# Performance work log

Hardware: AMD Instinct MI355X
Metric: run time of the kernel (lower is better)

## Reference

```python
import jax, jax.numpy as jnp
import numpy as np

B, S, H, NH = 4, 2048, 1024, 16
D = H // NH  # head dim = 64


def setup_inputs() -> dict:
    key = jax.random.key(0)
    ks = jax.random.split(key, 4)
    scale = 1.0 / np.sqrt(H)
    return {
        "hidden_states": jax.random.normal(ks[0], (B, S, H), dtype=jnp.float32),
        "attention_mask": jnp.zeros((B, 1, 1, S), dtype=jnp.float32),
        "Wq": jax.random.normal(ks[1], (H, H), dtype=jnp.float32) * scale,
        "bq": jnp.zeros((H,), dtype=jnp.float32),
        "Wk": jax.random.normal(ks[2], (H, H), dtype=jnp.float32) * scale,
        "bk": jnp.zeros((H,), dtype=jnp.float32),
        "Wv": jax.random.normal(ks[3], (H, H), dtype=jnp.float32) * scale,
        "bv": jnp.zeros((H,), dtype=jnp.float32),
    }


def _split_heads(x):
    # [B, S, H] -> [B, NH, S, D]
    return x.reshape(B, S, NH, D).transpose(0, 2, 1, 3)


def reference(hidden_states, attention_mask, Wq, bq, Wk, bk, Wv, bv):
    # NOTE: faithful to source quirk: key/value projections are applied to the
    # query projection output (mixed_query_layer), not to keyvalue_states.
    mixed_q = hidden_states @ Wq.T + bq            # [B, S, H]
    q = _split_heads(mixed_q)                       # [B, NH, S, D]
    k = _split_heads(mixed_q @ Wk.T + bk)           # [B, NH, S, D]
    v = _split_heads(mixed_q @ Wv.T + bv)           # [B, NH, S, D]

    scores = jnp.einsum("bhqd,bhkd->bhqk", q, k) / jnp.sqrt(jnp.float32(D))
    scores = scores + attention_mask                # additive mask [B,1,1,S]
    probs = jax.nn.softmax(scores, axis=-1)         # dropout = identity (eval)
    ctx = jnp.einsum("bhqk,bhkd->bhqd", probs, v)   # [B, NH, S, D]
    ctx = ctx.transpose(0, 2, 1, 3).reshape(B, S, H)
    return ctx
```

## Files before the change

### kernel.cpp

```cpp
#include <hip/hip_runtime.h>
#include <stdint.h>

typedef float  f32x4  __attribute__((ext_vector_type(4)));
typedef float  f32x16 __attribute__((ext_vector_type(16)));
typedef short  s16x8  __attribute__((ext_vector_type(8)));
typedef unsigned int u32x4 __attribute__((ext_vector_type(4)));
typedef unsigned short u16;
typedef u16    u16x4 __attribute__((ext_vector_type(4)));

#define SLEN 2048
#define HDIM 1024
#define NHEAD 16
#define DHEAD 64
#define BATCH 4
#define LOG2E 1.44269504088896340736f
#define SC2   0.18033688011111772f
#define ISC2  5.5451774444795623f

__device__ __forceinline__ u16 f2bf(float f) {
  uint32_t u = __builtin_bit_cast(uint32_t, f);
  u += 0x7FFFu + ((u >> 16) & 1u);
  return (u16)(u >> 16);
}

__device__ __forceinline__ uint32_t cvtpk2(float a, float b) {
  uint32_t r;
  asm("v_cvt_pk_bf16_f32 %0, %1, %2" : "=v"(r) : "v"(a), "v"(b));
  return r;
}

__device__ __forceinline__ void gld_lds16(const void* g, void* l) {
  __builtin_amdgcn_global_load_lds(
      (const __attribute__((address_space(1))) unsigned int*)g,
      (__attribute__((address_space(3))) unsigned int*)l, 16, 0, 0);
}

__global__ __launch_bounds__(256) void cvt_bf16(const float4* __restrict__ in,
                                                u16* __restrict__ out, int n4) {
  int i = blockIdx.x * 256 + threadIdx.x;
  if (i < n4) {
    float4 v = in[i];
    u16x4 o;
    o.x = f2bf(v.x); o.y = f2bf(v.y); o.z = f2bf(v.z); o.w = f2bf(v.w);
    *(u16x4*)(out + (size_t)i * 4) = o;
  }
}

__global__ __launch_bounds__(256) void cvt_w3(const float4* __restrict__ W0,
                                              const float4* __restrict__ W1,
                                              const float4* __restrict__ W2,
                                              u16* __restrict__ O0,
                                              u16* __restrict__ O1,
                                              u16* __restrict__ O2) {
  const float4* in = blockIdx.y == 0 ? W0 : (blockIdx.y == 1 ? W1 : W2);
  u16* out = blockIdx.y == 0 ? O0 : (blockIdx.y == 1 ? O1 : O2);
  const float sc = blockIdx.y == 0 ? SC2 : ISC2;
  int i = blockIdx.x * 256 + threadIdx.x;
  float4 v = in[i];
  u16x4 o;
  o.x = f2bf(v.x * sc); o.y = f2bf(v.y * sc);
  o.z = f2bf(v.z * sc); o.w = f2bf(v.w * sc);
  *(u16x4*)(out + (size_t)i * 4) = o;
}

__global__ __launch_bounds__(256) void prep_small(const float* __restrict__ mask,
                                                  const float* __restrict__ bq,
                                                  float* __restrict__ m2,
                                                  float* __restrict__ bqs) {
  int bid = blockIdx.x, tid = threadIdx.x;
  if (bid < 32) {
    int i = bid * 256 + tid;
    m2[i] = mask[i] * LOG2E;
  } else {
#pragma unroll
    for (int k = 0; k < 4; ++k) bqs[tid + k * 256] = bq[tid + k * 256] * SC2;
  }
}

__device__ __forceinline__ void gemm_body(const u16* __restrict__ A,
                                          const u16* __restrict__ W,
                                          const float* __restrict__ bias,
                                          u16* __restrict__ C, int mode) {
  __shared__ u16 As[128][32];
  __shared__ u16 Bs[128][32];
  const int tid = threadIdx.x;
  const int lane = tid & 63;
  const int w = tid >> 6;
  const int wr = w >> 1, wc = w & 1;
  const int brow = blockIdx.y * 128;
  const int bcol = blockIdx.x * 128;
  const int l15 = lane & 15, l4 = lane >> 4;
  const int koff = l4 * 8;

  f32x4 acc[4][4];
#pragma unroll
  for (int m = 0; m < 4; ++m)
#pragma unroll
    for (int n = 0; n < 4; ++n) acc[m][n] = f32x4{0.f, 0.f, 0.f, 0.f};

  for (int kt = 0; kt < HDIM / 32; ++kt) {
    __syncthreads();
#pragma unroll
    for (int it = 0; it < 2; ++it) {
      int c = tid + it * 256;
      int r = c >> 2, c4 = c & 3;
      gld_lds16(A + (size_t)(brow + r) * HDIM + kt * 32 + c4 * 8,
                (u16*)&As[0][0] + (size_t)c * 8);
      gld_lds16(W + (size_t)(bcol + r) * HDIM + kt * 32 + c4 * 8,
                (u16*)&Bs[0][0] + (size_t)c * 8);
    }
    __syncthreads();

    s16x8 af[4], bfr[4];
#pragma unroll
    for (int m = 0; m < 4; ++m)
      af[m] = *(const s16x8*)&As[wr * 64 + m * 16 + l15][koff];
#pragma unroll
    for (int n = 0; n < 4; ++n)
      bfr[n] = *(const s16x8*)&Bs[wc * 64 + n * 16 + l15][koff];
#pragma unroll
    for (int m = 0; m < 4; ++m)
#pragma unroll
      for (int n = 0; n < 4; ++n)
        acc[m][n] = __builtin_amdgcn_mfma_f32_16x16x32_bf16(af[m], bfr[n],
                                                            acc[m][n], 0, 0, 0);
  }

#pragma unroll
  for (int n = 0; n < 4; ++n) {
    int col = bcol + wc * 64 + n * 16 + l15;
    float bv = bias[col];
#pragma unroll
    for (int m = 0; m < 4; ++m) {
      int row0 = brow + wr * 64 + m * 16 + l4 * 4;
      if (mode == 0) {
#pragma unroll
        for (int j = 0; j < 4; ++j)
          C[(size_t)(row0 + j) * HDIM + col] = f2bf(acc[m][n][j] + bv);
      } else {
        u16x4 o;
#pragma unroll
        for (int j = 0; j < 4; ++j) o[j] = f2bf(acc[m][n][j] + bv);
        *(u16x4*)(C + (size_t)(((row0 >> 11) << 10) + col) * SLEN +
                  (row0 & (SLEN - 1))) = o;
      }
    }
  }
}

__global__ __launch_bounds__(256) void gemm_bt(const u16* __restrict__ A,
                                               const u16* __restrict__ W,
                                               const float* __restrict__ bias,
                                               u16* __restrict__ C) {
  gemm_body(A, W, bias, C, 0);
}

__global__ __launch_bounds__(256) void gemm_kv(const u16* __restrict__ A,
                                               const u16* __restrict__ Wk,
                                               const float* __restrict__ bk,
                                               u16* __restrict__ K,
                                               const u16* __restrict__ Wv,
                                               const float* __restrict__ bv,
                                               u16* __restrict__ Vt) {
  if (blockIdx.z == 0) gemm_body(A, Wk, bk, K, 0);
  else                 gemm_body(A, Wv, bv, Vt, 1);
}

__global__ __launch_bounds__(256, 4) void attn_kernel(
    const u16* __restrict__ Qs, const u16* __restrict__ Kb,
    const u16* __restrict__ Vtg, const float* __restrict__ m2g,
    float* __restrict__ out) {
  __shared__ u16 Ks[2][64 * 64];
  __shared__ u16 Vts[2][64 * 64];

  const int tid = threadIdx.x;
  const int lane = tid & 63;
  const int w = tid >> 6;
  const int bid = blockIdx.x;
  const int swz = (bid & 7) * 128 + (bid >> 3);
  const int qt = swz & 15;
  const int bh = swz >> 4;
  const int b = bh >> 4, h = bh & 15;
  const int l31 = lane & 31;
  const int h1 = lane >> 5;

  const int q0 = qt * 128 + w * 32;
  s16x8 qf[4];
  {
    const u16* qp = Qs + (size_t)(b * SLEN + q0 + l31) * HDIM + h * DHEAD + h1 * 8;
#pragma unroll
    for (int dch = 0; dch < 4; ++dch) qf[dch] = *(const s16x8*)(qp + dch * 16);
  }

  const int r0 = tid >> 3, c0 = tid & 7;
  const int cl0 = c0 ^ (r0 & 7);
  const int r1 = r0 + 32;
  const int cl1 = c0 ^ (r1 & 7);
  const u16* Kbase = Kb + (size_t)(b * SLEN) * HDIM + h * DHEAD;
  const u16* Vbase = Vtg + (size_t)bh * 64 * SLEN;
  const float* mbase = m2g + b * SLEN;

  f32x16 acc0{}, acc1{};
  float s_sm = 0.f;

  gld_lds16(Kbase + (size_t)r0 * HDIM + cl0 * 8, &Ks[0][0] + tid * 8);
  gld_lds16(Kbase + (size_t)r1 * HDIM + cl1 * 8, &Ks[0][0] + (tid + 256) * 8);
  gld_lds16(Vbase + (size_t)r0 * SLEN + cl0 * 8, &Vts[0][0] + tid * 8);
  gld_lds16(Vbase + (size_t)r1 * SLEN + cl1 * 8, &Vts[0][0] + (tid + 256) * 8);
  __syncthreads();

  int cur = 0;
  for (int kb = 0; kb < SLEN / 64; ++kb) {
    if (kb + 1 < SLEN / 64) {
      const int nb = (kb + 1) * 64;
      gld_lds16(Kbase + (size_t)(nb + r0) * HDIM + cl0 * 8,
                &Ks[cur ^ 1][0] + tid * 8);
      gld_lds16(Kbase + (size_t)(nb + r1) * HDIM + cl1 * 8,
                &Ks[cur ^ 1][0] + (tid + 256) * 8);
      gld_lds16(Vbase + (size_t)r0 * SLEN + nb + cl0 * 8,
                &Vts[cur ^ 1][0] + tid * 8);
      gld_lds16(Vbase + (size_t)r1 * SLEN + nb + cl1 * 8,
                &Vts[cur ^ 1][0] + (tid + 256) * 8);
    }
    const u16* Kc = &Ks[cur][0];
    const u16* Vc = &Vts[cur][0];

    uint32_t W[16];
#pragma unroll
    for (int kblk = 0; kblk < 2; ++kblk) {
      f32x16 sT{};
      __builtin_amdgcn_s_setprio(1);
#pragma unroll
      for (int dch = 0; dch < 4; ++dch) {
        const int row = kblk * 32 + l31;
        const int ch = (dch * 2 + h1) ^ (row & 7);
        s16x8 kf = *(const s16x8*)(Kc + row * 64 + ch * 8);
        sT = __builtin_amdgcn_mfma_f32_32x32x16_bf16(kf, qf[dch], sT, 0, 0, 0);
      }
      __builtin_amdgcn_s_setprio(0);
      float p[16];
      float ts = 0.f;
#pragma unroll
      for (int g = 0; g < 4; ++g) {
        float4 mk = *(const float4*)(mbase + kb * 64 + kblk * 32 + g * 8 + h1 * 4);
        p[4 * g + 0] = __builtin_amdgcn_exp2f(sT[4 * g + 0] + mk.x);
        p[4 * g + 1] = __builtin_amdgcn_exp2f(sT[4 * g + 1] + mk.y);
        p[4 * g + 2] = __builtin_amdgcn_exp2f(sT[4 * g + 2] + mk.z);
        p[4 * g + 3] = __builtin_amdgcn_exp2f(sT[4 * g + 3] + mk.w);
        ts += (p[4 * g + 0] + p[4 * g + 1]) + (p[4 * g + 2] + p[4 * g + 3]);
        W[kblk * 8 + 2 * g]     = cvtpk2(p[4 * g + 0], p[4 * g + 1]);
        W[kblk * 8 + 2 * g + 1] = cvtpk2(p[4 * g + 2], p[4 * g + 3]);
      }
      s_sm += ts;
    }

#pragma unroll
    for (int c = 0; c < 4; ++c) {
#pragma unroll
      for (int e = 0; e < 2; ++e) {
        uint32_t A = W[4 * c + e], B = W[4 * c + 2 + e];
        uint32_t v = h1 ? A : B;
        uint32_t cr = (uint32_t)__shfl_xor((int)v, 32);
        W[4 * c + e]     = h1 ? cr : A;
        W[4 * c + 2 + e] = h1 ? B : cr;
      }
    }

    __builtin_amdgcn_s_setprio(1);
#pragma unroll
    for (int c = 0; c < 4; ++c) {
      u32x4 t = {W[4 * c], W[4 * c + 1], W[4 * c + 2], W[4 * c + 3]};
      s16x8 af = __builtin_bit_cast(s16x8, t);
      const int ch = (c * 2 + h1) ^ (l31 & 7);
      s16x8 vf0 = *(const s16x8*)(Vc + l31 * 64 + ch * 8);
      s16x8 vf1 = *(const s16x8*)(Vc + (32 + l31) * 64 + ch * 8);
      acc0 = __builtin_amdgcn_mfma_f32_32x32x16_bf16(af, vf0, acc0, 0, 0, 0);
      acc1 = __builtin_amdgcn_mfma_f32_32x32x16_bf16(af, vf1, acc1, 0, 0, 0);
    }
    __builtin_amdgcn_s_setprio(0);

    __syncthreads();
    cur ^= 1;
  }

  s_sm += __shfl_xor(s_sm, 32);
  const float sinv = 1.0f / s_sm;
  const size_t obase = (size_t)(b * SLEN + q0);
#pragma unroll
  for (int r = 0; r < 16; ++r) {
    const int qr = (r & 3) + 8 * (r >> 2) + 4 * h1;
    const float si = __shfl(sinv, qr);
    float* op = out + (obase + qr) * HDIM + h * DHEAD;
    op[l31]      = acc0[r] * si;
    op[32 + l31] = acc1[r] * si;
  }
}

extern "C" void kernel_launch(void* const* d_in, const int* in_sizes, int n_in,
                              void* d_out, int out_size, void* d_ws, size_t ws_size,
                              hipStream_t stream) {
  (void)in_sizes; (void)n_in; (void)out_size; (void)ws_size;
  const float* hs   = (const float*)d_in[0];
  const float* mask = (const float*)d_in[1];
  const float* Wq   = (const float*)d_in[2];
  const float* bq   = (const float*)d_in[3];
  const float* Wk   = (const float*)d_in[4];
  const float* bk   = (const float*)d_in[5];
  const float* Wv   = (const float*)d_in[6];
  const float* bv   = (const float*)d_in[7];
  float* out = (float*)d_out;

  char* ws = (char*)d_ws;
  const size_t MTOK = (size_t)BATCH * SLEN;
  const size_t MB = 1024 * 1024;
  u16* HSb = (u16*)ws;
  u16* Wqs = (u16*)(ws + 16 * MB);
  u16* Wks = (u16*)(ws + 18 * MB);
  u16* Wvs = (u16*)(ws + 20 * MB);
  u16* Qs  = (u16*)(ws + 22 * MB);
  u16* Kb  = (u16*)(ws + 38 * MB);
  u16* Vt  = (u16*)(ws + 54 * MB);
  float* m2  = (float*)(ws + 70 * MB);
  float* bqs = m2 + MTOK;

  cvt_bf16<<<(int)(MTOK * HDIM / 4 / 256), 256, 0, stream>>>(
      (const float4*)hs, HSb, (int)(MTOK * HDIM / 4));
  dim3 gw(HDIM * HDIM / 4 / 256, 3);
  cvt_w3<<<gw, 256, 0, stream>>>((const float4*)Wq, (const float4*)Wk,
                                 (const float4*)Wv, Wqs, Wks, Wvs);
  prep_small<<<33, 256, 0, stream>>>(mask, bq, m2, bqs);

  dim3 gg(HDIM / 128, MTOK / 128);
  gemm_bt<<<gg, 256, 0, stream>>>(HSb, Wqs, bqs, Qs);
  dim3 gkv(HDIM / 128, MTOK / 128, 2);
  gemm_kv<<<gkv, 256, 0, stream>>>(Qs, Wks, bk, Kb, Wvs, bv, Vt);

  attn_kernel<<<BATCH * NHEAD * (SLEN / 128), 256, 0, stream>>>(Qs, Kb, Vt, m2,
                                                                out);
}
```

Baseline: 202.2 us.

## Merge prep kernels, deepen GEMM K-tile, fold mask into MFMA, use permlane swap

The three preprocessing kernels are merged into one launch, which saves two launch gaps. The projection GEMM now loads 64-wide K tiles, halving the number of barrier-separated iterations at the cost of larger LDS tiles without swizzling, so bank conflicts may increase. The attention kernel seeds the score accumulator with the mask so the add disappears from the exp path. The cross-half shuffle is replaced by v_permlane32_swap. These are several independent micro-optimizations.

```diff
diff --git a/kernel.cpp b/kernel.cpp
--- a/kernel.cpp
+++ b/kernel.cpp
@@ -35,45 +35,36 @@
       (__attribute__((address_space(3))) unsigned int*)l, 16, 0, 0);
 }
 
-__global__ __launch_bounds__(256) void cvt_bf16(const float4* __restrict__ in,
-                                                u16* __restrict__ out, int n4) {
-  int i = blockIdx.x * 256 + threadIdx.x;
-  if (i < n4) {
+__global__ __launch_bounds__(256) void prep_all(
+    const float4* __restrict__ hs, const float4* __restrict__ W0,
+    const float4* __restrict__ W1, const float4* __restrict__ W2,
+    const float* __restrict__ mask, const float* __restrict__ bq,
+    u16* __restrict__ HSb, u16* __restrict__ O0, u16* __restrict__ O1,
+    u16* __restrict__ O2, float* __restrict__ m2, float* __restrict__ bqs) {
+  const int bid = blockIdx.x, tid = threadIdx.x;
+  if (bid < 8192) {
+    int i = bid * 256 + tid;
+    float4 v = hs[i];
+    u16x4 o;
+    o.x = f2bf(v.x); o.y = f2bf(v.y); o.z = f2bf(v.z); o.w = f2bf(v.w);
+    *(u16x4*)(HSb + (size_t)i * 4) = o;
+  } else if (bid < 11264) {
+    int zz = (bid - 8192) >> 10;
+    int i = ((bid - 8192) & 1023) * 256 + tid;
+    const float4* in = zz == 0 ? W0 : (zz == 1 ? W1 : W2);
+    u16* out = zz == 0 ? O0 : (zz == 1 ? O1 : O2);
+    const float sc = zz == 0 ? SC2 : ISC2;
     float4 v = in[i];
     u16x4 o;
-    o.x = f2bf(v.x); o.y = f2bf(v.y); o.z = f2bf(v.z); o.w = f2bf(v.w);
+    o.x = f2bf(v.x * sc); o.y = f2bf(v.y * sc);
+    o.z = f2bf(v.z * sc); o.w = f2bf(v.w * sc);
     *(u16x4*)(out + (size_t)i * 4) = o;
-  }
-}
-
-__global__ __launch_bounds__(256) void cvt_w3(const float4* __restrict__ W0,
-                                              const float4* __restrict__ W1,
-                                              const float4* __restrict__ W2,
-                                              u16* __restrict__ O0,
-                                              u16* __restrict__ O1,
-                                              u16* __restrict__ O2) {
-  const float4* in = blockIdx.y == 0 ? W0 : (blockIdx.y == 1 ? W1 : W2);
-  u16* out = blockIdx.y == 0 ? O0 : (blockIdx.y == 1 ? O1 : O2);
-  const float sc = blockIdx.y == 0 ? SC2 : ISC2;
-  int i = blockIdx.x * 256 + threadIdx.x;
-  float4 v = in[i];
-  u16x4 o;
-  o.x = f2bf(v.x * sc); o.y = f2bf(v.y * sc);
-  o.z = f2bf(v.z * sc); o.w = f2bf(v.w * sc);
-  *(u16x4*)(out + (size_t)i * 4) = o;
-}
-
-__global__ __launch_bounds__(256) void prep_small(const float* __restrict__ mask,
-                                                  const float* __restrict__ bq,
-                                                  float* __restrict__ m2,
-                                                  float* __restrict__ bqs) {
-  int bid = blockIdx.x, tid = threadIdx.x;
-  if (bid < 32) {
-    int i = bid * 256 + tid;
+  } else if (bid < 11296) {
+    int i = (bid - 11264) * 256 + tid;
     m2[i] = mask[i] * LOG2E;
   } else {
-#pragma unroll
-    for (int k = 0; k < 4; ++k) bqs[tid + k * 256] = bq[tid + k * 256] * SC2;
+    int i = (bid - 11296) * 256 + tid;
+    if (i < HDIM) bqs[i] = bq[i] * SC2;
   }
 }
 
@@ -81,8 +72,8 @@
                                           const u16* __restrict__ W,
                                           const float* __restrict__ bias,
                                           u16* __restrict__ C, int mode) {
-  __shared__ u16 As[128][32];
-  __shared__ u16 Bs[128][32];
+  __shared__ u16 As[128 * 64];
+  __shared__ u16 Bs[128 * 64];
   const int tid = threadIdx.x;
   const int lane = tid & 63;
   const int w = tid >> 6;
@@ -98,32 +89,37 @@
 #pragma unroll
     for (int n = 0; n < 4; ++n) acc[m][n] = f32x4{0.f, 0.f, 0.f, 0.f};
 
-  for (int kt = 0; kt < HDIM / 32; ++kt) {
+  for (int kt = 0; kt < HDIM / 64; ++kt) {
     __syncthreads();
 #pragma unroll
-    for (int it = 0; it < 2; ++it) {
+    for (int it = 0; it < 4; ++it) {
       int c = tid + it * 256;
-      int r = c >> 2, c4 = c & 3;
-      gld_lds16(A + (size_t)(brow + r) * HDIM + kt * 32 + c4 * 8,
-                (u16*)&As[0][0] + (size_t)c * 8);
-      gld_lds16(W + (size_t)(bcol + r) * HDIM + kt * 32 + c4 * 8,
-                (u16*)&Bs[0][0] + (size_t)c * 8);
+      int r = c >> 3, c8 = c & 7;
+      gld_lds16(A + (size_t)(brow + r) * HDIM + kt * 64 + c8 * 8,
+                (u16*)As + (size_t)c * 8);
+      gld_lds16(W + (size_t)(bcol + r) * HDIM + kt * 64 + c8 * 8,
+                (u16*)Bs + (size_t)c * 8);
     }
     __syncthreads();
 
-    s16x8 af[4], bfr[4];
-#pragma unroll
-    for (int m = 0; m < 4; ++m)
-      af[m] = *(const s16x8*)&As[wr * 64 + m * 16 + l15][koff];
-#pragma unroll
-    for (int n = 0; n < 4; ++n)
-      bfr[n] = *(const s16x8*)&Bs[wc * 64 + n * 16 + l15][koff];
-#pragma unroll
-    for (int m = 0; m < 4; ++m)
+#pragma unroll
+    for (int kk = 0; kk < 2; ++kk) {
+      s16x8 af[4], bfr[4];
+#pragma unroll
+      for (int m = 0; m < 4; ++m)
+        af[m] = *(const s16x8*)(As + (size_t)(wr * 64 + m * 16 + l15) * 64 +
+                                kk * 32 + koff);
 #pragma unroll
       for (int n = 0; n < 4; ++n)
-        acc[m][n] = __builtin_amdgcn_mfma_f32_16x16x32_bf16(af[m], bfr[n],
-                                                            acc[m][n], 0, 0, 0);
+        bfr[n] = *(const s16x8*)(Bs + (size_t)(wc * 64 + n * 16 + l15) * 64 +
+                                 kk * 32 + koff);
+#pragma unroll
+      for (int m = 0; m < 4; ++m)
+#pragma unroll
+        for (int n = 0; n < 4; ++n)
+          acc[m][n] = __builtin_amdgcn_mfma_f32_16x16x32_bf16(af[m], bfr[n],
+                                                              acc[m][n], 0, 0, 0);
+    }
   }
 
 #pragma unroll
@@ -228,7 +224,13 @@
     uint32_t W[16];
 #pragma unroll
     for (int kblk = 0; kblk < 2; ++kblk) {
-      f32x16 sT{};
+      f32x16 sT;
+#pragma unroll
+      for (int g = 0; g < 4; ++g) {
+        float4 mk = *(const float4*)(mbase + kb * 64 + kblk * 32 + g * 8 + h1 * 4);
+        sT[4 * g + 0] = mk.x; sT[4 * g + 1] = mk.y;
+        sT[4 * g + 2] = mk.z; sT[4 * g + 3] = mk.w;
+      }
       __builtin_amdgcn_s_setprio(1);
 #pragma unroll
       for (int dch = 0; dch < 4; ++dch) {
@@ -238,18 +240,16 @@
         sT = __builtin_amdgcn_mfma_f32_32x32x16_bf16(kf, qf[dch], sT, 0, 0, 0);
       }
       __builtin_amdgcn_s_setprio(0);
-      float p[16];
       float ts = 0.f;
 #pragma unroll
       for (int g = 0; g < 4; ++g) {
-        float4 mk = *(const float4*)(mbase + kb * 64 + kblk * 32 + g * 8 + h1 * 4);
-        p[4 * g + 0] = __builtin_amdgcn_exp2f(sT[4 * g + 0] + mk.x);
-        p[4 * g + 1] = __builtin_amdgcn_exp2f(sT[4 * g + 1] + mk.y);
-        p[4 * g + 2] = __builtin_amdgcn_exp2f(sT[4 * g + 2] + mk.z);
-        p[4 * g + 3] = __builtin_amdgcn_exp2f(sT[4 * g + 3] + mk.w);
-        ts += (p[4 * g + 0] + p[4 * g + 1]) + (p[4 * g + 2] + p[4 * g + 3]);
-        W[kblk * 8 + 2 * g]     = cvtpk2(p[4 * g + 0], p[4 * g + 1]);
-        W[kblk * 8 + 2 * g + 1] = cvtpk2(p[4 * g + 2], p[4 * g + 3]);
+        float p0 = __builtin_amdgcn_exp2f(sT[4 * g + 0]);
+        float p1 = __builtin_amdgcn_exp2f(sT[4 * g + 1]);
+        float p2 = __builtin_amdgcn_exp2f(sT[4 * g + 2]);
+        float p3 = __builtin_amdgcn_exp2f(sT[4 * g + 3]);
+        ts += (p0 + p1) + (p2 + p3);
+        W[kblk * 8 + 2 * g]     = cvtpk2(p0, p1);
+        W[kblk * 8 + 2 * g + 1] = cvtpk2(p2, p3);
       }
       s_sm += ts;
     }
@@ -258,11 +258,10 @@
     for (int c = 0; c < 4; ++c) {
 #pragma unroll
       for (int e = 0; e < 2; ++e) {
-        uint32_t A = W[4 * c + e], B = W[4 * c + 2 + e];
-        uint32_t v = h1 ? A : B;
-        uint32_t cr = (uint32_t)__shfl_xor((int)v, 32);
-        W[4 * c + e]     = h1 ? cr : A;
-        W[4 * c + 2 + e] = h1 ? B : cr;
+        uint32_t a = W[4 * c + e], bb = W[4 * c + 2 + e];
+        asm("v_permlane32_swap_b32 %0, %1" : "+v"(a), "+v"(bb));
+        W[4 * c + e] = a;
+        W[4 * c + 2 + e] = bb;
       }
     }
 
@@ -323,12 +322,9 @@
   float* m2  = (float*)(ws + 70 * MB);
   float* bqs = m2 + MTOK;
 
-  cvt_bf16<<<(int)(MTOK * HDIM / 4 / 256), 256, 0, stream>>>(
-      (const float4*)hs, HSb, (int)(MTOK * HDIM / 4));
-  dim3 gw(HDIM * HDIM / 4 / 256, 3);
-  cvt_w3<<<gw, 256, 0, stream>>>((const float4*)Wq, (const float4*)Wk,
-                                 (const float4*)Wv, Wqs, Wks, Wvs);
-  prep_small<<<33, 256, 0, stream>>>(mask, bq, m2, bqs);
+  prep_all<<<11300, 256, 0, stream>>>((const float4*)hs, (const float4*)Wq,
+                                      (const float4*)Wk, (const float4*)Wv,
+                                      mask, bq, HSb, Wqs, Wks, Wvs, m2, bqs);
 
   dim3 gg(HDIM / 128, MTOK / 128);
   gemm_bt<<<gg, 256, 0, stream>>>(HSb, Wqs, bqs, Qs);
```

After: 190.7 us. -5.7%, faster.
